# Performance work log

Hardware: AMD Instinct MI355X
Metric: run time of the kernel (lower is better)

## Reference

```python
import jax, jax.numpy as jnp
import numpy as np

N = 50000
NUM_GRAPHS = 64
EPS = 1e-16  # PyG softmax denominator epsilon


def _gat_conv(x, src, dst, W, a_src, a_dst, b, heads, out_ch):
    n = x.shape[0]
    h = (x @ W).reshape(n, heads, out_ch)                    # [N,H,C]
    al_s = jnp.einsum('nhc,hc->nh', h, a_src)                # [N,H]
    al_d = jnp.einsum('nhc,hc->nh', h, a_dst)                # [N,H]
    e = jax.nn.leaky_relu(al_s[src] + al_d[dst], 0.2)        # [E,H]
    emax = jax.ops.segment_max(e, dst, num_segments=n)       # [N,H]
    ee = jnp.exp(e - emax[dst])
    den = jax.ops.segment_sum(ee, dst, num_segments=n)       # [N,H]
    alpha = ee / (den[dst] + EPS)                            # [E,H]
    msg = h[src] * alpha[:, :, None]                         # [E,H,C]
    out = jax.ops.segment_sum(msg, dst, num_segments=n)      # [N,H,C]
    return out.reshape(n, heads * out_ch) + b


def setup_inputs() -> dict:
    key = jax.random.key(0)
    ks = jax.random.split(key, 16)
    E = 250000
    x = jax.random.normal(ks[0], (N, 11), dtype=jnp.float32)
    edge_index = jax.random.randint(ks[1], (2, E), 0, N, dtype=jnp.int64)
    batch = jnp.sort(jax.random.randint(ks[2], (N,), 0, NUM_GRAPHS, dtype=jnp.int64))
    def glorot(k, shape):
        fan = shape[0] + shape[-1]
        return jax.random.uniform(k, shape, jnp.float32, -1.0, 1.0) * np.sqrt(6.0 / fan)
    return {
        'x': x, 'edge_index': edge_index, 'batch': batch,
        'W1': glorot(ks[3], (11, 8 * 128)),
        'a1s': glorot(ks[4], (8, 128)), 'a1d': glorot(ks[5], (8, 128)),
        'b1': jnp.zeros((8 * 128,), jnp.float32),
        'W2': glorot(ks[6], (1024, 8 * 64)),
        'a2s': glorot(ks[7], (8, 64)), 'a2d': glorot(ks[8], (8, 64)),
        'b2': jnp.zeros((8 * 64,), jnp.float32),
        'W3': glorot(ks[9], (512, 4 * 32)),
        'a3s': glorot(ks[10], (4, 32)), 'a3d': glorot(ks[11], (4, 32)),
        'b3': jnp.zeros((4 * 32,), jnp.float32),
        'Wout': glorot(ks[12], (128, 1)),
        'bout': jnp.zeros((1,), jnp.float32),
    }


def reference(x, edge_index, batch, W1, a1s, a1d, b1, W2, a2s, a2d, b2,
              W3, a3s, a3d, b3, Wout, bout):
    n = x.shape[0]
    # GATConv adds self-loops by default
    loop = jnp.arange(n, dtype=edge_index.dtype)
    src = jnp.concatenate([edge_index[0], loop])
    dst = jnp.concatenate([edge_index[1], loop])
    h = jax.nn.leaky_relu(_gat_conv(x, src, dst, W1, a1s, a1d, b1, 8, 128), 0.01)
    h = jax.nn.leaky_relu(_gat_conv(h, src, dst, W2, a2s, a2d, b2, 8, 64), 0.01)
    h = jax.nn.leaky_relu(_gat_conv(h, src, dst, W3, a3s, a3d, b3, 4, 32), 0.01)
    # global mean pool over graphs
    sums = jax.ops.segment_sum(h, batch, num_segments=NUM_GRAPHS)      # [G,128]
    cnt = jax.ops.segment_sum(jnp.ones((n,), h.dtype), batch, num_segments=NUM_GRAPHS)
    pooled = sums / jnp.maximum(cnt, 1.0)[:, None]
    return pooled @ Wout + bout                                        # [G,1]
```

## Files before the change

### kernel.cpp

```cpp
#include <hip/hip_runtime.h>

#define EPS 1e-16f

typedef __attribute__((ext_vector_type(8))) short short8;
typedef __attribute__((ext_vector_type(4))) float f32x4;

__device__ __forceinline__ float b2f(unsigned short u) {
    return __uint_as_float(((unsigned)u) << 16);
}
__device__ __forceinline__ unsigned short f2b(float f) {
    unsigned u = __float_as_uint(f);
    u += 0x7fffu + ((u >> 16) & 1u);
    return (unsigned short)(u >> 16);
}

typedef __attribute__((address_space(3))) void lds_vp;
typedef __attribute__((address_space(1))) const void glb_vp;
__device__ __forceinline__ void load_lds16(const unsigned short* g,
                                           unsigned short* l) {
    __builtin_amdgcn_global_load_lds((glb_vp*)g, (lds_vp*)l, 16, 0, 0);
}

__global__ void init_deg_kernel(int* deg, int N) {
    int i = blockIdx.x * blockDim.x + threadIdx.x;
    if (i < N) deg[i] = 1;
}

__global__ void hist_kernel(const int* __restrict__ ei, int E, int N, int* deg) {
    int e = blockIdx.x * blockDim.x + threadIdx.x;
    if (e < E) {
        int d = ei[E + e];
        if ((unsigned)d < (unsigned)N) atomicAdd(&deg[d], 1);
    }
}

__global__ void scan_block_kernel(const int* __restrict__ deg,
                                  int* __restrict__ rowst,
                                  int* __restrict__ bsum, int N) {
    __shared__ int s[256];
    int t = threadIdx.x, b = blockIdx.x;
    int i = b * 256 + t;
    s[t] = (i < N) ? deg[i] : 0;
    __syncthreads();
    for (int o = 1; o < 256; o <<= 1) {
        int a = (t >= o) ? s[t - o] : 0;
        __syncthreads();
        s[t] += a;
        __syncthreads();
    }
    if (i < N) rowst[i + 1] = s[t];
    if (t == 255) bsum[b] = s[255];
}

__global__ void scan_top_kernel(const int* __restrict__ bsum,
                                int* __restrict__ boff, int NB) {
    __shared__ int psum[65];
    int t = threadIdx.x;
    int chunk = (NB + 63) / 64;
    int lo = t * chunk, hi = lo + chunk;
    if (lo > NB) lo = NB;
    if (hi > NB) hi = NB;
    int s = 0;
    for (int i = lo; i < hi; i++) s += bsum[i];
    psum[t + 1] = s;
    __syncthreads();
    if (t == 0) {
        psum[0] = 0;
        for (int i = 1; i <= 64; i++) psum[i] += psum[i - 1];
    }
    __syncthreads();
    int run = psum[t];
    for (int i = lo; i < hi; i++) {
        boff[i] = run;
        run += bsum[i];
    }
}

__global__ void scan_finish_kernel(int* __restrict__ rowst,
                                   const int* __restrict__ boff,
                                   const int* __restrict__ deg,
                                   int* __restrict__ srcs,
                                   int* __restrict__ cursor, int N) {
    int i = blockIdx.x * 256 + threadIdx.x;
    if (i == 0) rowst[0] = 0;
    if (i < N) {
        int incl = rowst[i + 1] + boff[blockIdx.x];
        rowst[i + 1] = incl;
        int st = incl - deg[i];
        srcs[st] = i;
        cursor[i] = st + 1;
    }
}

__global__ void scatter_kernel(const int* __restrict__ ei, int E, int N,
                               int* cursor, int* srcs) {
    int e = blockIdx.x * blockDim.x + threadIdx.x;
    if (e < E) {
        int d = ei[E + e];
        if ((unsigned)d < (unsigned)N) {
            int p = atomicAdd(&cursor[d], 1);
            int s = ei[e];
            if ((unsigned)s >= (unsigned)N) s = d;
            srcs[p] = s;
        }
    }
}

__global__ void wprep_kernel(const float* __restrict__ W1,
                             const float* __restrict__ W2,
                             const float* __restrict__ W3,
                             unsigned short* __restrict__ wt2,
                             unsigned short* __restrict__ wt3,
                             unsigned short* __restrict__ w1sk) {
    int i = blockIdx.x * blockDim.x + threadIdx.x;
    if (i < 1024 * 512) {
        int k = i / 512, n = i % 512;
        wt2[(size_t)n * 1024 + k] = f2b(W2[i]);
    } else if (i < 1024 * 512 + 512 * 128) {
        int j = i - 1024 * 512;
        int k = j / 128, n = j % 128;
        wt3[(size_t)n * 512 + k] = f2b(W3[j]);
    } else if (i < 1024 * 512 + 512 * 128 + 8 * 128 * 32) {
        int q = i - (1024 * 512 + 512 * 128);
        int h = q >> 12, rem = q & 4095;
        int c = rem >> 5, kk = rem & 31;
        int off = (h == 7) ? 16 : 0;
        float v = 0.f;
        int k = kk - off;
        if (k >= 0 && k < 11) v = W1[k * 1024 + h * 128 + c];
        w1sk[q] = f2b(v);
    }
}

__global__ void wa1_kernel(const float* __restrict__ W1,
                           const float* __restrict__ a1s,
                           const float* __restrict__ a1d,
                           float* __restrict__ w_as, float* __restrict__ w_ad) {
    int t = threadIdx.x;
    if (t >= 88) return;
    int h = t / 11, k = t % 11;
    float s = 0.f, d = 0.f;
    for (int c = 0; c < 128; c++) {
        float w = W1[k * 1024 + h * 128 + c];
        s += w * a1s[h * 128 + c];
        d += w * a1d[h * 128 + c];
    }
    w_as[h * 16 + k] = s;
    w_ad[h * 16 + k] = d;
}

__global__ void al1_kernel(const float* __restrict__ x,
                           const float* __restrict__ w_as,
                           const float* __restrict__ w_ad,
                           float* __restrict__ als, float* __restrict__ ald,
                           int N) {
    int i = blockIdx.x * blockDim.x + threadIdx.x;
    if (i >= N * 8) return;
    int n = i >> 3, h = i & 7;
    float s = 0.f, d = 0.f;
#pragma unroll
    for (int k = 0; k < 11; k++) {
        float xv = x[n * 11 + k];
        s += xv * w_as[h * 16 + k];
        d += xv * w_ad[h * 16 + k];
    }
    als[i] = s;
    ald[i] = d;
}

__global__ void agg1_fused(const float* __restrict__ x,
                           const float* __restrict__ als,
                           const float* __restrict__ ald,
                           const int* __restrict__ rowst,
                           const int* __restrict__ srcs,
                           unsigned short* __restrict__ A2, int N) {
    constexpr int MAXE = 64;
    __shared__ float sv[MAXE * 8];
    __shared__ int ssrc[MAXE];
    int n = blockIdx.x;
    int t = threadIdx.x;
    int h = t >> 4, k = t & 15;
    int start = rowst[n], end = rowst[n + 1];
    int deg = end - start;
    float acc = 0.f;

    if (deg <= MAXE) {
        for (int p = t; p < deg * 8; p += 128) {
            int e = p >> 3, hh = p & 7;
            int s = srcs[start + e];
            if (hh == 0) ssrc[e] = s;
            float v = als[s * 8 + hh] + ald[n * 8 + hh];
            sv[e * 8 + hh] = v > 0.f ? v : 0.2f * v;
        }
        __syncthreads();
        float m = -1e30f;
        for (int e = k; e < deg; e += 16) m = fmaxf(m, sv[e * 8 + h]);
#pragma unroll
        for (int o = 1; o < 16; o <<= 1) m = fmaxf(m, __shfl_xor(m, o));
        float ee[(MAXE + 15) / 16];
        float den = 0.f;
        {
            int kk = 0;
            for (int e = k; e < deg; e += 16, kk++) {
                float xv = expf(sv[e * 8 + h] - m);
                ee[kk] = xv;
                den += xv;
            }
        }
#pragma unroll
        for (int o = 1; o < 16; o <<= 1) den += __shfl_xor(den, o);
        float dinv = 1.0f / (den + EPS);
        {
            int kk = 0;
            for (int e = k; e < deg; e += 16, kk++)
                sv[e * 8 + h] = ee[kk] * dinv;
        }
        __syncthreads();
        const int CH = 4;
        for (int e = 0; e < deg; e += CH) {
            int mc = deg - e;
            if (mc > CH) mc = CH;
            int ss[CH];
            float al[CH], xv[CH];
#pragma unroll
            for (int j = 0; j < CH; j++)
                if (j < mc) {
                    ss[j] = ssrc[e + j];
                    al[j] = sv[(e + j) * 8 + h];
                }
#pragma unroll
            for (int j = 0; j < CH; j++)
                if (j < mc) xv[j] = (k < 11) ? x[ss[j] * 11 + k] : 0.f;
#pragma unroll
            for (int j = 0; j < CH; j++)
                if (j < mc) acc += al[j] * xv[j];
        }
    } else {
        float aldn = ald[n * 8 + h];
        float m = -1e30f;
        for (int idx = start + k; idx < end; idx += 16) {
            float v = als[srcs[idx] * 8 + h] + aldn;
            v = v > 0.f ? v : 0.2f * v;
            m = fmaxf(m, v);
        }
#pragma unroll
        for (int o = 1; o < 16; o <<= 1) m = fmaxf(m, __shfl_xor(m, o));
        float den = 0.f;
        for (int idx = start + k; idx < end; idx += 16) {
            float v = als[srcs[idx] * 8 + h] + aldn;
            v = v > 0.f ? v : 0.2f * v;
            den += expf(v - m);
        }
#pragma unroll
        for (int o = 1; o < 16; o <<= 1) den += __shfl_xor(den, o);
        float dinv = 1.0f / (den + EPS);
        for (int idx = start; idx < end; idx++) {
            int s = srcs[idx];
            float v = als[s * 8 + h] + aldn;
            v = v > 0.f ? v : 0.2f * v;
            float a = expf(v - m) * dinv;
            float xv = (k < 11) ? x[s * 11 + k] : 0.f;
            acc += a * xv;
        }
    }
    A2[(size_t)n * 128 + t] = f2b(acc);
}

template <bool EPI, int HB, int CC, bool SK>
__global__ __launch_bounds__(256) void gemm_mfma(
    const unsigned short* __restrict__ A, const unsigned short* __restrict__ Bt,
    unsigned short* __restrict__ C, const float* __restrict__ bias,
    const float* __restrict__ a_s, const float* __restrict__ a_d,
    float* __restrict__ als, float* __restrict__ ald, int H, int M, int N,
    int K, int lda) {
    int NX = gridDim.x;
    int bid = blockIdx.y * NX + blockIdx.x;
    int win = bid & (8 * NX - 1);
    int mg = bid / (8 * NX);
    int m_t = mg * 8 + (win & 7);
    int n_t = win >> 3;
    int bm = m_t * 128, bn = n_t * 128;
    if (bm >= M) return;

    union SMem {
        struct {
            unsigned short As[2][128 * 32];
            unsigned short Bs[2][128 * 32];
        } k;
        unsigned short Ct[128 * 132];
    };
    __shared__ __align__(16) SMem sm;
    auto& As = sm.k.As;
    auto& Bs = sm.k.Bs;
    auto& Ct = sm.Ct;

    int t = threadIdx.x;
    int w = t >> 6, lane = t & 63;
    int quad = lane >> 4, l16 = lane & 15;
    int wr = (w >> 1) * 64, wc = (w & 1) * 64;

    int kofs = 0;
    const unsigned short* Bb = Bt;
    if (SK) {
        kofs = n_t * 16;
        if (kofs > lda - 32) kofs = lda - 32;
        Bb = Bt + (size_t)n_t * 128 * 32;
    }

    int c0 = w * 128 + lane;
    int c1 = c0 + 64;
    int r0 = c0 >> 2, p0 = c0 & 3;
    int r1 = c1 >> 2, p1 = c1 & 3;
    int j0 = (p0 - (r0 >> 1)) & 3;
    int j1 = (p1 - (r1 >> 1)) & 3;
    int ga0 = bm + r0;
    if (ga0 >= M) ga0 = M - 1;
    int ga1 = bm + r1;
    if (ga1 >= M) ga1 = M - 1;
    const unsigned short* Ag0 = A + (size_t)ga0 * lda + kofs + j0 * 8;
    const unsigned short* Ag1 = A + (size_t)ga1 * lda + kofs + j1 * 8;
    size_t br0 = SK ? (size_t)r0 : (size_t)(bn + r0);
    size_t br1 = SK ? (size_t)r1 : (size_t)(bn + r1);
    const unsigned short* Bg0 = Bb + br0 * K + j0 * 8;
    const unsigned short* Bg1 = Bb + br1 * K + j1 * 8;

    auto stage = [&](int st, int k0) {
        load_lds16(Ag0 + k0, &As[st][(w * 128) * 8]);
        load_lds16(Ag1 + k0, &As[st][(w * 128 + 64) * 8]);
        load_lds16(Bg0 + k0, &Bs[st][(w * 128) * 8]);
        load_lds16(Bg1 + k0, &Bs[st][(w * 128 + 64) * 8]);
    };

    int aoff[4], boff4[4];
#pragma unroll
    for (int i = 0; i < 4; i++) {
        int ra = wr + i * 16 + l16;
        aoff[i] = ra * 32 + (((quad + (ra >> 1)) & 3) * 8);
        int rb = wc + i * 16 + l16;
        boff4[i] = rb * 32 + (((quad + (rb >> 1)) & 3) * 8);
    }

    f32x4 acc[4][4] = {};
    stage(0, 0);
    int st = 0;
    for (int k0 = 0; k0 < K; k0 += 32, st ^= 1) {
        __syncthreads();
        if (k0 + 32 < K) stage(st ^ 1, k0 + 32);
        short8 a[4], b[4];
#pragma unroll
        for (int mi = 0; mi < 4; mi++) a[mi] = *(const short8*)&As[st][aoff[mi]];
#pragma unroll
        for (int ni = 0; ni < 4; ni++) b[ni] = *(const short8*)&Bs[st][boff4[ni]];
#pragma unroll
        for (int mi = 0; mi < 4; mi++)
#pragma unroll
            for (int ni = 0; ni < 4; ni++)
                acc[mi][ni] = __builtin_amdgcn_mfma_f32_16x16x32_bf16(
                    a[mi], b[ni], acc[mi][ni], 0, 0, 0);
    }
    __syncthreads();

#pragma unroll
    for (int mi = 0; mi < 4; mi++) {
#pragma unroll
        for (int r = 0; r < 4; r++) {
            int rl = wr + mi * 16 + quad * 4 + r;
#pragma unroll
            for (int ni = 0; ni < 4; ni++) {
                int cl = wc + ni * 16 + l16;
                float v = acc[mi][ni][r];
                if (EPI) {
                    v += bias[bn + cl];
                    v = v > 0.f ? v : 0.01f * v;
                }
                Ct[rl * 132 + cl] = f2b(v);
            }
        }
    }
    __syncthreads();
#pragma unroll
    for (int p = 0; p < 16; p++) {
        int q = p * 256 + t;
        int row = q >> 5, c8 = q & 31;
        if (bm + row < M) {
            uint2 v = *(const uint2*)&Ct[row * 132 + c8 * 4];
            *(uint2*)&C[(size_t)(bm + row) * N + bn + c8 * 4] = v;
        }
    }
    if (HB > 0) {
        for (int pi = t; pi < 128 * HB; pi += 256) {
            int row = pi / HB, hl = pi % HB;
            if (bm + row >= M) continue;
            int hg = bn / CC + hl;
            const unsigned short* rp = &Ct[row * 132 + hl * CC];
            const float* asp = a_s + hg * CC;
            const float* adp = a_d + hg * CC;
            float s = 0.f, d = 0.f;
#pragma unroll
            for (int c = 0; c < CC; c++) {
                float v = b2f(rp[c]);
                s += v * asp[c];
                d += v * adp[c];
            }
            als[(size_t)(bm + row) * H + hg] = s;
            ald[(size_t)(bm + row) * H + hg] = d;
        }
    }
}

template <int HB, int CC>
__global__ __launch_bounds__(256, 2) void gemm_pipe(
    const unsigned short* __restrict__ A, const unsigned short* __restrict__ Bt,
    unsigned short* __restrict__ C, const float* __restrict__ a_s,
    const float* __restrict__ a_d, float* __restrict__ als,
    float* __restrict__ ald, int H, int M, int N, int K) {
    int NX = gridDim.x;
    int bid = blockIdx.y * NX + blockIdx.x;
    int win = bid & (8 * NX - 1);
    int mg = bid / (8 * NX);
    int m_t = mg * 8 + (win & 7);
    int n_t = win >> 3;
    int bm = m_t * 128, bn = n_t * 128;
    if (bm >= M) return;

    union SMem {
        struct {
            unsigned short As[2][128 * 64];
            unsigned short Bs[2][128 * 64];
        } k;
        unsigned short Ct[128 * 132];
    };
    __shared__ __align__(16) SMem sm;

    int t = threadIdx.x;
    int w = t >> 6, lane = t & 63;
    int quad = lane >> 4, l16 = lane & 15;
    int wr = (w >> 1) * 64, wc = (w & 1) * 64;

    int srow = lane >> 3;
    int gsl = (lane & 7) ^ srow;
    const unsigned short* Ag[4];
    const unsigned short* Bg[4];
#pragma unroll
    for (int j = 0; j < 4; j++) {
        int row = (j * 4 + w) * 8 + srow;
        int ga = bm + row;
        if (ga > M - 1) ga = M - 1;
        Ag[j] = A + (size_t)ga * K + gsl * 8;
        Bg[j] = Bt + (size_t)(bn + row) * K + gsl * 8;
    }
    auto stage = [&](int st, int kt) {
        int ko = kt * 64;
#pragma unroll
        for (int j = 0; j < 4; j++) {
            load_lds16(Ag[j] + ko, &sm.k.As[st][(j * 4 + w) * 512]);
            load_lds16(Bg[j] + ko, &sm.k.Bs[st][(j * 4 + w) * 512]);
        }
    };

    int arow[4], brow[4];
#pragma unroll
    for (int i = 0; i < 4; i++) {
        arow[i] = (wr + i * 16 + l16) * 64;
        brow[i] = (wc + i * 16 + l16) * 64;
    }
    int sw = l16 & 7;

    f32x4 acc[4][4] = {};
    int NT = K >> 6;
    stage(0, 0);
    if (NT > 1) stage(1, 1);
    for (int tt = 0; tt < NT; tt++) {
        int bb = tt & 1;
        if (tt + 1 < NT)
            asm volatile("s_waitcnt vmcnt(8)" ::: "memory");
        else
            asm volatile("s_waitcnt vmcnt(0)" ::: "memory");
        __builtin_amdgcn_s_barrier();
        __builtin_amdgcn_sched_barrier(0);
#pragma unroll
        for (int ks = 0; ks < 2; ks++) {
            short8 a[4], b[4];
            int so = ((ks * 4 + quad) ^ sw) * 8;
#pragma unroll
            for (int mi = 0; mi < 4; mi++)
                a[mi] = *(const short8*)&sm.k.As[bb][arow[mi] + so];
#pragma unroll
            for (int ni = 0; ni < 4; ni++)
                b[ni] = *(const short8*)&sm.k.Bs[bb][brow[ni] + so];
            __builtin_amdgcn_s_setprio(1);
#pragma unroll
            for (int mi = 0; mi < 4; mi++)
#pragma unroll
                for (int ni = 0; ni < 4; ni++)
                    acc[mi][ni] = __builtin_amdgcn_mfma_f32_16x16x32_bf16(
                        a[mi], b[ni], acc[mi][ni], 0, 0, 0);
            __builtin_amdgcn_s_setprio(0);
        }
        asm volatile("s_waitcnt lgkmcnt(0)" ::: "memory");
        __builtin_amdgcn_s_barrier();
        if (tt + 2 < NT) stage(bb, tt + 2);
    }
    __syncthreads();

#pragma unroll
    for (int mi = 0; mi < 4; mi++) {
#pragma unroll
        for (int r = 0; r < 4; r++) {
            int rl = wr + mi * 16 + quad * 4 + r;
#pragma unroll
            for (int ni = 0; ni < 4; ni++) {
                int cl = wc + ni * 16 + l16;
                sm.Ct[rl * 132 + cl] = f2b(acc[mi][ni][r]);
            }
        }
    }
    __syncthreads();
#pragma unroll
    for (int p = 0; p < 16; p++) {
        int q = p * 256 + t;
        int row = q >> 5, c8 = q & 31;
        if (bm + row < M) {
            uint2 v = *(const uint2*)&sm.Ct[row * 132 + c8 * 4];
            *(uint2*)&C[(size_t)(bm + row) * N + bn + c8 * 4] = v;
        }
    }
    if (HB > 0) {
        for (int pi = t; pi < 128 * HB; pi += 256) {
            int row = pi / HB, hl = pi % HB;
            if (bm + row >= M) continue;
            int hg = bn / CC + hl;
            const unsigned short* rp = &sm.Ct[row * 132 + hl * CC];
            const float* asp = a_s + hg * CC;
            const float* adp = a_d + hg * CC;
            float s = 0.f, d = 0.f;
#pragma unroll
            for (int c = 0; c < CC; c++) {
                float v = b2f(rp[c]);
                s += v * asp[c];
                d += v * adp[c];
            }
            als[(size_t)(bm + row) * H + hg] = s;
            ald[(size_t)(bm + row) * H + hg] = d;
        }
    }
}

template <int H, int C>
__global__ void agg_fused4(const unsigned short* __restrict__ hin,
                           const float* __restrict__ als,
                           const float* __restrict__ ald,
                           const int* __restrict__ rowst,
                           const int* __restrict__ srcs,
                           const float* __restrict__ bias,
                           unsigned short* __restrict__ out, int N) {
    constexpr int HC = H * C;
    constexpr int NT = HC / 4;
    constexpr int TPH = C / 4;
    constexpr int MAXE = 64;
    __shared__ float sv[MAXE * H];
    __shared__ int ssrc[MAXE];
    int n = blockIdx.x;
    int t = threadIdx.x;
    int c = t * 4;
    int hh = c / C;
    int li = (c % C) / 4;
    int start = rowst[n], end = rowst[n + 1];
    int deg = end - start;
    float a0 = 0.f, a1 = 0.f, a2 = 0.f, a3 = 0.f;

    if (deg <= MAXE) {
        for (int p = t; p < deg * H; p += NT) {
            int e = p / H, h = p % H;
            int s = srcs[start + e];
            if (h == 0) ssrc[e] = s;
            float v = als[s * H + h] + ald[n * H + h];
            sv[e * H + h] = v > 0.f ? v : 0.2f * v;
        }
        __syncthreads();
        float m = -1e30f;
        for (int e = li; e < deg; e += TPH) m = fmaxf(m, sv[e * H + hh]);
#pragma unroll
        for (int o = 1; o < TPH; o <<= 1) m = fmaxf(m, __shfl_xor(m, o));
        float ee[(MAXE + TPH - 1) / TPH];
        float den = 0.f;
        {
            int k = 0;
            for (int e = li; e < deg; e += TPH, k++) {
                float x = expf(sv[e * H + hh] - m);
                ee[k] = x;
                den += x;
            }
        }
#pragma unroll
        for (int o = 1; o < TPH; o <<= 1) den += __shfl_xor(den, o);
        float dinv = 1.0f / (den + EPS);
        {
            int k = 0;
            for (int e = li; e < deg; e += TPH, k++)
                sv[e * H + hh] = ee[k] * dinv;
        }
        __syncthreads();
        const int CH = 4;
        for (int e = 0; e < deg; e += CH) {
            int mc = deg - e;
            if (mc > CH) mc = CH;
            int ss[CH];
            float al[CH];
            ushort4 uv[CH];
#pragma unroll
            for (int j = 0; j < CH; j++)
                if (j < mc) {
                    ss[j] = ssrc[e + j];
                    al[j] = sv[(e + j) * H + hh];
                }
#pragma unroll
            for (int j = 0; j < CH; j++)
                if (j < mc)
                    uv[j] = *(const ushort4*)(hin + (size_t)ss[j] * HC + c);
#pragma unroll
            for (int j = 0; j < CH; j++)
                if (j < mc) {
                    a0 += al[j] * b2f(uv[j].x);
                    a1 += al[j] * b2f(uv[j].y);
                    a2 += al[j] * b2f(uv[j].z);
                    a3 += al[j] * b2f(uv[j].w);
                }
        }
    } else {
        float aldn = ald[n * H + hh];
        float m = -1e30f;
        for (int idx = start + li; idx < end; idx += TPH) {
            float v = als[srcs[idx] * H + hh] + aldn;
            v = v > 0.f ? v : 0.2f * v;
            m = fmaxf(m, v);
        }
#pragma unroll
        for (int o = 1; o < TPH; o <<= 1) m = fmaxf(m, __shfl_xor(m, o));
        float den = 0.f;
        for (int idx = start + li; idx < end; idx += TPH) {
            float v = als[srcs[idx] * H + hh] + aldn;
            v = v > 0.f ? v : 0.2f * v;
            den += expf(v - m);
        }
#pragma unroll
        for (int o = 1; o < TPH; o <<= 1) den += __shfl_xor(den, o);
        float dinv = 1.0f / (den + EPS);
        const int CH = 4;
        for (int idx = start; idx < end; idx += CH) {
            int mc = end - idx;
            if (mc > CH) mc = CH;
            int ss[CH];
            float lv[CH];
            ushort4 uv[CH];
#pragma unroll
            for (int j = 0; j < CH; j++)
                if (j < mc) ss[j] = srcs[idx + j];
#pragma unroll
            for (int j = 0; j < CH; j++)
                if (j < mc) lv[j] = als[ss[j] * H + hh];
#pragma unroll
            for (int j = 0; j < CH; j++)
                if (j < mc)
                    uv[j] = *(const ushort4*)(hin + (size_t)ss[j] * HC + c);
#pragma unroll
            for (int j = 0; j < CH; j++)
                if (j < mc) {
                    float v = lv[j] + aldn;
                    v = v > 0.f ? v : 0.2f * v;
                    float a = expf(v - m) * dinv;
                    a0 += a * b2f(uv[j].x);
                    a1 += a * b2f(uv[j].y);
                    a2 += a * b2f(uv[j].z);
                    a3 += a * b2f(uv[j].w);
                }
        }
    }
    float v0 = a0 + bias[c], v1 = a1 + bias[c + 1];
    float v2 = a2 + bias[c + 2], v3 = a3 + bias[c + 3];
    ushort4 o;
    o.x = f2b(v0 > 0.f ? v0 : 0.01f * v0);
    o.y = f2b(v1 > 0.f ? v1 : 0.01f * v1);
    o.z = f2b(v2 > 0.f ? v2 : 0.01f * v2);
    o.w = f2b(v3 > 0.f ? v3 : 0.01f * v3);
    *(ushort4*)&out[(size_t)n * HC + c] = o;
}

template <int H, int C>
__global__ void agg_fused2(const unsigned short* __restrict__ hin,
                           const float* __restrict__ als,
                           const float* __restrict__ ald,
                           const int* __restrict__ rowst,
                           const int* __restrict__ srcs,
                           const float* __restrict__ bias,
                           unsigned short* __restrict__ out, int N) {
    constexpr int HC = H * C;
    constexpr int NT = HC / 2;
    constexpr int TPH = C / 2;
    constexpr int MAXE = 64;
    __shared__ float sv[MAXE * H];
    __shared__ int ssrc[MAXE];
    int n = blockIdx.x;
    int t = threadIdx.x;
    int c = t * 2;
    int hh = c / C;
    int li = (c % C) / 2;
    int start = rowst[n], end = rowst[n + 1];
    int deg = end - start;
    float a0 = 0.f, a1 = 0.f;

    if (deg <= MAXE) {
        for (int p = t; p < deg * H; p += NT) {
            int e = p / H, h = p % H;
            int s = srcs[start + e];
            if (h == 0) ssrc[e] = s;
            float v = als[s * H + h] + ald[n * H + h];
            sv[e * H + h] = v > 0.f ? v : 0.2f * v;
        }
        __syncthreads();
        float m = -1e30f;
        for (int e = li; e < deg; e += TPH) m = fmaxf(m, sv[e * H + hh]);
#pragma unroll
        for (int o = 1; o < TPH; o <<= 1) m = fmaxf(m, __shfl_xor(m, o));
        float ee[(MAXE + TPH - 1) / TPH];
        float den = 0.f;
        {
            int k = 0;
            for (int e = li; e < deg; e += TPH, k++) {
                float x = expf(sv[e * H + hh] - m);
                ee[k] = x;
                den += x;
            }
        }
#pragma unroll
        for (int o = 1; o < TPH; o <<= 1) den += __shfl_xor(den, o);
        float dinv = 1.0f / (den + EPS);
        {
            int k = 0;
            for (int e = li; e < deg; e += TPH, k++)
                sv[e * H + hh] = ee[k] * dinv;
        }
        __syncthreads();
        const int CH = 4;
        for (int e = 0; e < deg; e += CH) {
            int mc = deg - e;
            if (mc > CH) mc = CH;
            int ss[CH];
            float al[CH];
            ushort2 uv[CH];
#pragma unroll
            for (int j = 0; j < CH; j++)
                if (j < mc) {
                    ss[j] = ssrc[e + j];
                    al[j] = sv[(e + j) * H + hh];
                }
#pragma unroll
            for (int j = 0; j < CH; j++)
                if (j < mc)
                    uv[j] = *(const ushort2*)(hin + (size_t)ss[j] * HC + c);
#pragma unroll
            for (int j = 0; j < CH; j++)
                if (j < mc) {
                    a0 += al[j] * b2f(uv[j].x);
                    a1 += al[j] * b2f(uv[j].y);
                }
        }
    } else {
        float aldn = ald[n * H + hh];
        float m = -1e30f;
        for (int idx = start + li; idx < end; idx += TPH) {
            float v = als[srcs[idx] * H + hh] + aldn;
            v = v > 0.f ? v : 0.2f * v;
            m = fmaxf(m, v);
        }
#pragma unroll
        for (int o = 1; o < TPH; o <<= 1) m = fmaxf(m, __shfl_xor(m, o));
        float den = 0.f;
        for (int idx = start + li; idx < end; idx += TPH) {
            float v = als[srcs[idx] * H + hh] + aldn;
            v = v > 0.f ? v : 0.2f * v;
            den += expf(v - m);
        }
#pragma unroll
        for (int o = 1; o < TPH; o <<= 1) den += __shfl_xor(den, o);
        float dinv = 1.0f / (den + EPS);
        const int CH = 4;
        for (int idx = start; idx < end; idx += CH) {
            int mc = end - idx;
            if (mc > CH) mc = CH;
            int ss[CH];
            float lv[CH];
            ushort2 uv[CH];
#pragma unroll
            for (int j = 0; j < CH; j++)
                if (j < mc) ss[j] = srcs[idx + j];
#pragma unroll
            for (int j = 0; j < CH; j++)
                if (j < mc) lv[j] = als[ss[j] * H + hh];
#pragma unroll
            for (int j = 0; j < CH; j++)
                if (j < mc)
                    uv[j] = *(const ushort2*)(hin + (size_t)ss[j] * HC + c);
#pragma unroll
            for (int j = 0; j < CH; j++)
                if (j < mc) {
                    float v = lv[j] + aldn;
                    v = v > 0.f ? v : 0.2f * v;
                    float a = expf(v - m) * dinv;
                    a0 += a * b2f(uv[j].x);
                    a1 += a * b2f(uv[j].y);
                }
        }
    }
    float v0 = a0 + bias[c], v1 = a1 + bias[c + 1];
    ushort2 o;
    o.x = f2b(v0 > 0.f ? v0 : 0.01f * v0);
    o.y = f2b(v1 > 0.f ? v1 : 0.01f * v1);
    *(ushort2*)&out[(size_t)n * HC + c] = o;
}

__global__ void pool_init_kernel(float* pool, int GC) {
    int i = blockIdx.x * blockDim.x + threadIdx.x;
    if (i < GC) pool[i] = 0.f;
}

__global__ void pool_partial_kernel(const unsigned short* __restrict__ h3,
                                    const int* __restrict__ batch,
                                    float* __restrict__ pool, int N, int G) {
    int lo = blockIdx.x * 128;
    int hi = lo + 128;
    if (hi > N) hi = N;
    if (lo >= N) return;
    int t = threadIdx.x;
    int cur = batch[lo];
    float acc = 0.f;
    for (int n = lo; n < hi; n++) {
        int g = batch[n];
        if (g != cur) {
            if ((unsigned)cur < (unsigned)G) atomicAdd(&pool[cur * 128 + t], acc);
            acc = 0.f;
            cur = g;
        }
        acc += b2f(h3[(size_t)n * 128 + t]);
    }
    if ((unsigned)cur < (unsigned)G) atomicAdd(&pool[cur * 128 + t], acc);
}

__global__ void head_kernel(const float* __restrict__ pool,
                            const int* __restrict__ batch,
                            const float* __restrict__ Wout,
                            const float* __restrict__ bout,
                            float* __restrict__ out, int N) {
    int g = blockIdx.x;
    int t = threadIdx.x;
    int lo, hi;
    {
        int a = 0, b = N;
        while (a < b) { int mid = (a + b) >> 1; if (batch[mid] < g) a = mid + 1; else b = mid; }
        lo = a;
        a = lo; b = N;
        while (a < b) { int mid = (a + b) >> 1; if (batch[mid] < g + 1) a = mid + 1; else b = mid; }
        hi = a;
    }
    float c = (float)(hi - lo);
    c = c > 1.f ? c : 1.f;
    float v = (pool[g * 128 + t] / c) * Wout[t];
    for (int o = 32; o; o >>= 1) v += __shfl_xor(v, o);
    __shared__ float partial[2];
    if ((t & 63) == 0) partial[t >> 6] = v;
    __syncthreads();
    if (t == 0) out[g] = partial[0] + partial[1] + bout[0];
}

extern "C" void kernel_launch(void* const* d_in, const int* in_sizes, int n_in,
                              void* d_out, int out_size, void* d_ws,
                              size_t ws_size, hipStream_t stream) {
    const float* x = (const float*)d_in[0];
    const int* ei = (const int*)d_in[1];
    const int* batch = (const int*)d_in[2];
    const float* W1 = (const float*)d_in[3];
    const float* a1s = (const float*)d_in[4];
    const float* a1d = (const float*)d_in[5];
    const float* b1 = (const float*)d_in[6];
    const float* W2 = (const float*)d_in[7];
    const float* a2s = (const float*)d_in[8];
    const float* a2d = (const float*)d_in[9];
    const float* b2 = (const float*)d_in[10];
    const float* W3 = (const float*)d_in[11];
    const float* a3s = (const float*)d_in[12];
    const float* a3d = (const float*)d_in[13];
    const float* b3 = (const float*)d_in[14];
    const float* Wout = (const float*)d_in[15];
    const float* bout = (const float*)d_in[16];
    float* out = (float*)d_out;

    const int N = in_sizes[0] / 11;
    const int E = in_sizes[1] / 2;
    const int Etot = E + N;
    const int G = out_size;
    const int NB = (N + 255) / 256;
    const int MT = ((N + 127) / 128 + 7) / 8 * 8;

    char* ws = (char*)d_ws;
    size_t off = 0;
    auto alloc = [&](size_t bytes) -> void* {
        void* p = ws + off;
        off += (bytes + 255) & ~(size_t)255;
        return p;
    };
    unsigned short* buf1 = (unsigned short*)alloc((size_t)N * 1024 * 2);
    unsigned short* buf2 = (unsigned short*)alloc((size_t)N * 1024 * 2);
    float* als = (float*)alloc((size_t)N * 8 * 4);
    float* ald = (float*)alloc((size_t)N * 8 * 4);
    int* rowst = (int*)alloc((size_t)(N + 1) * 4);
    int* cursor = (int*)alloc((size_t)N * 4);
    int* srcs = (int*)alloc((size_t)Etot * 4);
    int* deg = (int*)alloc((size_t)N * 4);
    int* bsum = (int*)alloc((size_t)NB * 4);
    int* boff = (int*)alloc((size_t)NB * 4);
    float* pool = (float*)alloc((size_t)G * 128 * 4);
    unsigned short* aggx = (unsigned short*)alloc((size_t)N * 128 * 2);
    unsigned short* w1sk = (unsigned short*)alloc((size_t)8 * 128 * 32 * 2);
    unsigned short* wt2 = (unsigned short*)alloc((size_t)1024 * 512 * 2);
    unsigned short* wt3 = (unsigned short*)alloc((size_t)512 * 128 * 2);
    float* w_as = (float*)alloc(8 * 16 * 4);
    float* w_ad = (float*)alloc(8 * 16 * 4);

    int nb = (N + 255) / 256;
    int eb = (E + 255) / 256;

    init_deg_kernel<<<nb, 256, 0, stream>>>(deg, N);
    hist_kernel<<<eb, 256, 0, stream>>>(ei, E, N, deg);
    scan_block_kernel<<<NB, 256, 0, stream>>>(deg, rowst, bsum, N);
    scan_top_kernel<<<1, 64, 0, stream>>>(bsum, boff, NB);
    scan_finish_kernel<<<NB, 256, 0, stream>>>(rowst, boff, deg, srcs, cursor,
                                               N);
    scatter_kernel<<<eb, 256, 0, stream>>>(ei, E, N, cursor, srcs);

    const int WTOT = 1024 * 512 + 512 * 128 + 8 * 128 * 32;
    wprep_kernel<<<(WTOT + 255) / 256, 256, 0, stream>>>(W1, W2, W3, wt2, wt3,
                                                         w1sk);
    wa1_kernel<<<1, 128, 0, stream>>>(W1, a1s, a1d, w_as, w_ad);

    al1_kernel<<<(N * 8 + 255) / 256, 256, 0, stream>>>(x, w_as, w_ad, als, ald,
                                                        N);
    agg1_fused<<<N, 128, 0, stream>>>(x, als, ald, rowst, srcs, aggx, N);
    gemm_mfma<true, 0, 1, true><<<dim3(8, MT), 256, 0, stream>>>(
        aggx, w1sk, buf2, b1, nullptr, nullptr, nullptr, nullptr, 0, N, 1024,
        32, 128);

    gemm_pipe<2, 64><<<dim3(4, MT), 256, 0, stream>>>(
        buf2, wt2, buf1, a2s, a2d, als, ald, 8, N, 512, 1024);
    agg_fused4<8, 64><<<N, 128, 0, stream>>>(buf1, als, ald, rowst, srcs, b2,
                                             buf2, N);

    gemm_pipe<4, 32><<<dim3(1, MT), 256, 0, stream>>>(
        buf2, wt3, buf1, a3s, a3d, als, ald, 4, N, 128, 512);
    agg_fused2<4, 32><<<N, 64, 0, stream>>>(buf1, als, ald, rowst, srcs, b3,
                                            buf2, N);

    pool_init_kernel<<<(G * 128 + 255) / 256, 256, 0, stream>>>(pool, G * 128);
    pool_partial_kernel<<<(N + 127) / 128, 128, 0, stream>>>(buf2, batch, pool,
                                                             N, G);
    head_kernel<<<G, 128, 0, stream>>>(pool, batch, Wout, bout, out, N);
}
```

Baseline: 447.3 us.

## Use 256x256-tile 512-thread GEMM with XCD-aware block mapping for layer 2

Replaces the layer-2 128x128 pipelined GEMM with a new kernel that computes 256x256 output tiles using 8 waves, each holding an 8x4 grid of MFMA accumulators. The larger tiles raise arithmetic intensity and cut how often A and B are re-read from memory. Block IDs are remapped so consecutive tiles land on the same XCD, which is meant to improve L2 locality. The attention-logit epilogue is kept, done in two 128-row halves through LDS. The trade-off is more registers and LDS per block, which may lower occupancy, and a coarser grid of only about 392 blocks.

```diff
diff --git a/kernel.cpp b/kernel.cpp
--- a/kernel.cpp
+++ b/kernel.cpp
@@ -408,6 +408,151 @@
     }
 }
 
+__global__ __launch_bounds__(512, 2) void gemm_l2(
+    const unsigned short* __restrict__ A, const unsigned short* __restrict__ Bt,
+    unsigned short* __restrict__ C, const float* __restrict__ a_s,
+    const float* __restrict__ a_d, float* __restrict__ als,
+    float* __restrict__ ald, int H, int M, int N, int K) {
+    int nnt = N >> 8;
+    int nwg = gridDim.x;
+    int bid = blockIdx.x;
+    int q = nwg >> 3, r = nwg & 7;
+    int xcd = bid & 7, idx = bid >> 3;
+    int base = (xcd < r) ? xcd * (q + 1) : r * (q + 1) + (xcd - r) * q;
+    int swz = base + idx;
+    int m_t = swz / nnt, n_t = swz % nnt;
+    int bm = m_t * 256, bn = n_t * 256;
+    if (bm >= M) return;
+
+    union SMem {
+        struct {
+            unsigned short As[2][256 * 64];
+            unsigned short Bs[2][256 * 64];
+        } k;
+        unsigned short Ct[128 * 264];
+    };
+    __shared__ __align__(16) SMem sm;
+
+    int t = threadIdx.x;
+    int w = t >> 6, lane = t & 63;
+    int quad = lane >> 4, l16 = lane & 15;
+    int wm = w >> 2, wn = w & 3;
+    int wr = wm * 128, wc = wn * 64;
+
+    int srow = lane >> 3;
+    int gsl = (lane & 7) ^ srow;
+    const unsigned short* Ag[4];
+    const unsigned short* Bg[4];
+#pragma unroll
+    for (int j = 0; j < 4; j++) {
+        int row = j * 64 + w * 8 + srow;
+        int ga = bm + row;
+        if (ga > M - 1) ga = M - 1;
+        Ag[j] = A + (size_t)ga * K + gsl * 8;
+        Bg[j] = Bt + (size_t)(bn + row) * K + gsl * 8;
+    }
+    auto stage = [&](int st, int kt) {
+        int ko = kt * 64;
+#pragma unroll
+        for (int j = 0; j < 4; j++) {
+            load_lds16(Ag[j] + ko, &sm.k.As[st][(j * 512 + w * 64) * 8]);
+            load_lds16(Bg[j] + ko, &sm.k.Bs[st][(j * 512 + w * 64) * 8]);
+        }
+    };
+
+    int arow[8], brow[4];
+#pragma unroll
+    for (int i = 0; i < 8; i++) arow[i] = (wr + i * 16 + l16) * 64;
+#pragma unroll
+    for (int i = 0; i < 4; i++) brow[i] = (wc + i * 16 + l16) * 64;
+    int sw = l16 & 7;
+
+    f32x4 acc[8][4] = {};
+    int NT = K >> 6;
+    stage(0, 0);
+    stage(1, 1);
+    for (int tt = 0; tt < NT; tt++) {
+        int bb = tt & 1;
+        if (tt + 1 < NT)
+            asm volatile("s_waitcnt vmcnt(8)" ::: "memory");
+        else
+            asm volatile("s_waitcnt vmcnt(0)" ::: "memory");
+        __builtin_amdgcn_s_barrier();
+        __builtin_amdgcn_sched_barrier(0);
+#pragma unroll
+        for (int ks = 0; ks < 2; ks++) {
+            short8 a[8], b[4];
+            int so = ((ks * 4 + quad) ^ sw) * 8;
+#pragma unroll
+            for (int ni = 0; ni < 4; ni++)
+                b[ni] = *(const short8*)&sm.k.Bs[bb][brow[ni] + so];
+#pragma unroll
+            for (int mi = 0; mi < 8; mi++)
+                a[mi] = *(const short8*)&sm.k.As[bb][arow[mi] + so];
+            __builtin_amdgcn_s_setprio(1);
+#pragma unroll
+            for (int mi = 0; mi < 8; mi++)
+#pragma unroll
+                for (int ni = 0; ni < 4; ni++)
+                    acc[mi][ni] = __builtin_amdgcn_mfma_f32_16x16x32_bf16(
+                        a[mi], b[ni], acc[mi][ni], 0, 0, 0);
+            __builtin_amdgcn_s_setprio(0);
+        }
+        asm volatile("s_waitcnt lgkmcnt(0)" ::: "memory");
+        __builtin_amdgcn_s_barrier();
+        if (tt + 2 < NT) stage(bb, tt + 2);
+    }
+    __syncthreads();
+
+    for (int h = 0; h < 2; h++) {
+        if (wm == h) {
+#pragma unroll
+            for (int mi = 0; mi < 8; mi++) {
+#pragma unroll
+                for (int rr = 0; rr < 4; rr++) {
+                    int rl = mi * 16 + quad * 4 + rr;
+#pragma unroll
+                    for (int ni = 0; ni < 4; ni++) {
+                        int cl = wc + ni * 16 + l16;
+                        sm.Ct[rl * 264 + cl] = f2b(acc[mi][ni][rr]);
+                    }
+                }
+            }
+        }
+        __syncthreads();
+#pragma unroll
+        for (int p = 0; p < 8; p++) {
+            int qq = p * 512 + t;
+            int row = qq >> 5, c8 = qq & 31;
+            int gr = bm + h * 128 + row;
+            if (gr < M) {
+                uint4 v = *(const uint4*)&sm.Ct[row * 264 + c8 * 8];
+                *(uint4*)&C[(size_t)gr * N + bn + c8 * 8] = v;
+            }
+        }
+        {
+            int row = t >> 2, hl = t & 3;
+            int gr = bm + h * 128 + row;
+            if (gr < M) {
+                int hg = (bn >> 6) + hl;
+                const unsigned short* rp = &sm.Ct[row * 264 + hl * 64];
+                const float* asp = a_s + hg * 64;
+                const float* adp = a_d + hg * 64;
+                float s = 0.f, d = 0.f;
+#pragma unroll
+                for (int c = 0; c < 64; c++) {
+                    float v = b2f(rp[c]);
+                    s += v * asp[c];
+                    d += v * adp[c];
+                }
+                als[(size_t)gr * H + hg] = s;
+                ald[(size_t)gr * H + hg] = d;
+            }
+        }
+        __syncthreads();
+    }
+}
+
 template <int HB, int CC>
 __global__ __launch_bounds__(256, 2) void gemm_pipe(
     const unsigned short* __restrict__ A, const unsigned short* __restrict__ Bt,
@@ -900,6 +1045,7 @@
     const int G = out_size;
     const int NB = (N + 255) / 256;
     const int MT = ((N + 127) / 128 + 7) / 8 * 8;
+    const int MT256 = (N + 255) / 256;
 
     char* ws = (char*)d_ws;
     size_t off = 0;
@@ -949,8 +1095,8 @@
         aggx, w1sk, buf2, b1, nullptr, nullptr, nullptr, nullptr, 0, N, 1024,
         32, 128);
 
-    gemm_pipe<2, 64><<<dim3(4, MT), 256, 0, stream>>>(
-        buf2, wt2, buf1, a2s, a2d, als, ald, 8, N, 512, 1024);
+    gemm_l2<<<MT256 * 2, 512, 0, stream>>>(buf2, wt2, buf1, a2s, a2d, als, ald,
+                                           8, N, 512, 1024);
     agg_fused4<8, 64><<<N, 128, 0, stream>>>(buf1, als, ald, rowst, srcs, b2,
                                              buf2, N);
 
```

After: 461.7 us. 1.03x slower.
